# Optimization experiments

Measured on AMD Instinct MI355X. Metric: run time of the kernel, lower is better.

## Reference

```python
import jax, jax.numpy as jnp
import numpy as np

N_NODES = 100000
N_EDGES = 400000
D = 128           # vector_dim
N_GRAPHS = 4096
N_LAYERS = 5
IN_FEAT = 11


def setup_inputs() -> dict:
    key = jax.random.key(0)
    ks = jax.random.split(key, 6)
    x = jax.random.uniform(ks[0], (N_NODES, IN_FEAT), dtype=jnp.float32)
    edge_index = jax.random.randint(ks[1], (2, N_EDGES), 0, N_NODES, dtype=jnp.int64)
    batch = jnp.sort(jax.random.randint(ks[2], (N_NODES,), 0, N_GRAPHS, dtype=jnp.int64))
    # expansion Linear(11, D)
    We = jax.random.normal(ks[3], (IN_FEAT, D), dtype=jnp.float32) * (1.0 / np.sqrt(IN_FEAT))
    be = jnp.zeros((D,), dtype=jnp.float32)
    # stacked GCNConv weights/biases for 5 layers
    Wg = jax.random.normal(ks[4], (N_LAYERS, D, D), dtype=jnp.float32) * (1.0 / np.sqrt(D))
    bg = jnp.zeros((N_LAYERS, D), dtype=jnp.float32)
    return {"x": x, "edge_index": edge_index, "batch": batch, "num_graphs": N_GRAPHS,
            "We": We, "be": be, "Wg": Wg, "bg": bg}


def reference(x, edge_index, batch, num_graphs, We, be, Wg, bg):
    n = x.shape[0]
    src, dst = edge_index[0], edge_index[1]
    # GCNConv(improved=True): self-loop weight 2 -> deg[i] = in_degree + 2
    deg = jax.ops.segment_sum(jnp.ones((src.shape[0],), x.dtype), dst, num_segments=n) + 2.0
    dinv = deg ** -0.5
    enorm = dinv[src] * dinv[dst]          # per-edge symmetric norm [E]
    self_norm = 2.0 * dinv * dinv          # self-loop contribution [N]

    h = jnp.log(x + 1.0) @ We + be         # expansion [N, D]
    for l in range(Wg.shape[0]):
        t = h @ Wg[l]                      # [N, D]
        agg = jax.ops.segment_sum(t[src] * enorm[:, None], dst, num_segments=n)
        agg = agg + self_norm[:, None] * t + bg[l]
        h = h + jax.nn.relu(agg)           # residual; dropout = identity (eval)
    return jax.ops.segment_sum(h, batch, num_segments=num_graphs)  # global_add_pool [G, D]
```

## Files before the change

### kernel.cpp

```cpp
#include <hip/hip_runtime.h>
#include <hip/hip_bf16.h>

#define NN 100000
#define NE 400000
#define DD 128
#define NG 4096
#define NL 5
#define NF 11


__global__ void deg_kernel(const int* __restrict__ ei, int* __restrict__ deg) {
    int e = blockIdx.x * 256 + threadIdx.x;
    if (e < NE) atomicAdd(&deg[ei[NE + e]], 1);
}

__global__ void scan1_kernel(const int* __restrict__ deg, int* __restrict__ off,
                             int* __restrict__ bsums) {
    __shared__ int lds[256];
    int tid = threadIdx.x, b = blockIdx.x;
    int base = b * 1024 + tid * 4;
    int v[4];
#pragma unroll
    for (int q = 0; q < 4; ++q) {
        int i = base + q;
        v[q] = (i < NN) ? deg[i] : 0;
    }
    int s = v[0] + v[1] + v[2] + v[3];
    lds[tid] = s;
    __syncthreads();
    for (int o = 1; o < 256; o <<= 1) {
        int t2 = (tid >= o) ? lds[tid - o] : 0;
        __syncthreads();
        lds[tid] += t2;
        __syncthreads();
    }
    int p = lds[tid] - s;
#pragma unroll
    for (int q = 0; q < 4; ++q) {
        int i = base + q;
        if (i < NN) off[i] = p;
        p += v[q];
    }
    if (tid == 255) bsums[b] = lds[255];
}

__global__ void scan2_kernel(int* __restrict__ bsums, int nb) {
    __shared__ int lds[128];
    int tid = threadIdx.x;
    int v = (tid < nb) ? bsums[tid] : 0;
    lds[tid] = v;
    __syncthreads();
    for (int o = 1; o < 128; o <<= 1) {
        int t2 = (tid >= o) ? lds[tid - o] : 0;
        __syncthreads();
        lds[tid] += t2;
        __syncthreads();
    }
    if (tid < nb) bsums[tid] = lds[tid] - v;
}

__global__ void finish_kernel(int* __restrict__ off, const int* __restrict__ bsums,
                              const int* __restrict__ deg, float* __restrict__ dinv) {
    int i = blockIdx.x * 256 + threadIdx.x;
    if (i == 0) off[NN] = NE;
    if (i < NN) {
        off[i] += bsums[i >> 10];
        dinv[i] = rsqrtf((float)deg[i] + 2.0f);
    }
}

__global__ void fill_kernel(const int* __restrict__ ei, const int* __restrict__ off,
                            int* __restrict__ cursor, int2* __restrict__ csr,
                            const float* __restrict__ dinv) {
    int e = blockIdx.x * 256 + threadIdx.x;
    if (e >= NE) return;
    int s = ei[e];
    int d = ei[NE + e];
    int pos = off[d] + atomicAdd(&cursor[d], 1);
    csr[pos] = make_int2(s, __float_as_int(dinv[s] * dinv[d]));
}


__global__ void expand_kernel(const float* __restrict__ x, const float* __restrict__ We,
                              const float* __restrict__ be, float* __restrict__ h) {
    int t = blockIdx.x * 256 + threadIdx.x;
    int i = t >> 7, j = t & 127;
    float acc = be[j];
#pragma unroll
    for (int f = 0; f < NF; ++f) {
        acc += __logf(x[i * NF + f] + 1.0f) * We[f * DD + j];
    }
    h[t] = acc;
}


__global__ __launch_bounds__(256) void layer_kernel(const float* __restrict__ hin,
                                                    float* __restrict__ hout,
                                                    const int* __restrict__ off,
                                                    const int2* __restrict__ csr,
                                                    const float* __restrict__ dinv,
                                                    const float* __restrict__ W,
                                                    const float* __restrict__ b) {
    __shared__ float gs[64 * 132];
    __shared__ float ws[2][8 * 128];
    const int tid = threadIdx.x;
    const int node0 = blockIdx.x * 64;
    const float4* __restrict__ h4 = (const float4*)hin;

    const int jj = tid & 31;
    const int sub = tid >> 5;
#pragma unroll 1
    for (int p = 0; p < 8; ++p) {
        const int nl = p * 8 + sub;
        const int node = node0 + nl;
        float4 acc = make_float4(0.f, 0.f, 0.f, 0.f);
        if (node < NN) {
            float di = dinv[node];
            float sn = 2.0f * di * di;
            float4 hv = h4[(size_t)node * 32 + jj];
            acc = make_float4(sn * hv.x, sn * hv.y, sn * hv.z, sn * hv.w);
            int e = off[node];
            const int e1 = off[node + 1];
            for (; e + 4 <= e1; e += 4) {
                int2 p0 = csr[e], p1 = csr[e + 1], p2 = csr[e + 2], p3 = csr[e + 3];
                float4 v0 = h4[(size_t)p0.x * 32 + jj];
                float4 v1 = h4[(size_t)p1.x * 32 + jj];
                float4 v2 = h4[(size_t)p2.x * 32 + jj];
                float4 v3 = h4[(size_t)p3.x * 32 + jj];
                float w0 = __int_as_float(p0.y), w1 = __int_as_float(p1.y);
                float w2 = __int_as_float(p2.y), w3 = __int_as_float(p3.y);
                acc.x = fmaf(w0, v0.x, acc.x); acc.y = fmaf(w0, v0.y, acc.y);
                acc.z = fmaf(w0, v0.z, acc.z); acc.w = fmaf(w0, v0.w, acc.w);
                acc.x = fmaf(w1, v1.x, acc.x); acc.y = fmaf(w1, v1.y, acc.y);
                acc.z = fmaf(w1, v1.z, acc.z); acc.w = fmaf(w1, v1.w, acc.w);
                acc.x = fmaf(w2, v2.x, acc.x); acc.y = fmaf(w2, v2.y, acc.y);
                acc.z = fmaf(w2, v2.z, acc.z); acc.w = fmaf(w2, v2.w, acc.w);
                acc.x = fmaf(w3, v3.x, acc.x); acc.y = fmaf(w3, v3.y, acc.y);
                acc.z = fmaf(w3, v3.z, acc.z); acc.w = fmaf(w3, v3.w, acc.w);
            }
            for (; e < e1; ++e) {
                int2 pe = csr[e];
                float4 v = h4[(size_t)pe.x * 32 + jj];
                float w = __int_as_float(pe.y);
                acc.x = fmaf(w, v.x, acc.x); acc.y = fmaf(w, v.y, acc.y);
                acc.z = fmaf(w, v.z, acc.z); acc.w = fmaf(w, v.w, acc.w);
            }
        }
        *(float4*)&gs[nl * 132 + jj * 4] = acc;
    }

    {
        float4 wv = *(const float4*)(W + tid * 4);
        *(float4*)&ws[0][tid * 4] = wv;
    }

    const int cg = tid & 15;
    const int rg = tid >> 4;
    float acc[4][8];
#pragma unroll
    for (int m = 0; m < 4; ++m)
#pragma unroll
        for (int q = 0; q < 8; ++q) acc[m][q] = 0.f;

#pragma unroll 1
    for (int kc = 0; kc < 16; ++kc) {
        const int cur = kc & 1;
        float4 wnext;
        const bool have = (kc + 1 < 16);
        if (have) wnext = *(const float4*)(W + (kc + 1) * 1024 + tid * 4);
        __syncthreads();
#pragma unroll
        for (int kk = 0; kk < 8; ++kk) {
            const float* wrow = &ws[cur][kk * 128];
            float4 wlo = *(const float4*)(wrow + cg * 4);
            float4 whi = *(const float4*)(wrow + cg * 4 + 64);
            const int k = kc * 8 + kk;
#pragma unroll
            for (int m = 0; m < 4; ++m) {
                float gv = gs[(rg + (m << 4)) * 132 + k];
                acc[m][0] = fmaf(gv, wlo.x, acc[m][0]);
                acc[m][1] = fmaf(gv, wlo.y, acc[m][1]);
                acc[m][2] = fmaf(gv, wlo.z, acc[m][2]);
                acc[m][3] = fmaf(gv, wlo.w, acc[m][3]);
                acc[m][4] = fmaf(gv, whi.x, acc[m][4]);
                acc[m][5] = fmaf(gv, whi.y, acc[m][5]);
                acc[m][6] = fmaf(gv, whi.z, acc[m][6]);
                acc[m][7] = fmaf(gv, whi.w, acc[m][7]);
            }
        }
        if (have) *(float4*)&ws[cur ^ 1][tid * 4] = wnext;
    }

    float4 blo = *(const float4*)(b + cg * 4);
    float4 bhi = *(const float4*)(b + cg * 4 + 64);
#pragma unroll
    for (int m = 0; m < 4; ++m) {
        int r = rg + (m << 4);
        int row = node0 + r;
        if (row < NN) {
            size_t o = (size_t)row * DD + cg * 4;
            float4 hlo = *(const float4*)(hin + o);
            float4 hhi = *(const float4*)(hin + o + 64);
            hlo.x += fmaxf(acc[m][0] + blo.x, 0.f);
            hlo.y += fmaxf(acc[m][1] + blo.y, 0.f);
            hlo.z += fmaxf(acc[m][2] + blo.z, 0.f);
            hlo.w += fmaxf(acc[m][3] + blo.w, 0.f);
            hhi.x += fmaxf(acc[m][4] + bhi.x, 0.f);
            hhi.y += fmaxf(acc[m][5] + bhi.y, 0.f);
            hhi.z += fmaxf(acc[m][6] + bhi.z, 0.f);
            hhi.w += fmaxf(acc[m][7] + bhi.w, 0.f);
            *(float4*)(hout + o) = hlo;
            *(float4*)(hout + o + 64) = hhi;
        }
    }
}


__global__ void pool_kernel(const float* __restrict__ h, const int* __restrict__ batch,
                            float* __restrict__ out) {
    int j = threadIdx.x;
    int n0 = blockIdx.x * 64;
    float acc = 0.f;
    int prev = -1;
    for (int n = 0; n < 64; ++n) {
        int i = n0 + n;
        if (i >= NN) break;
        int bi = batch[i];
        if (bi != prev) {
            if (prev >= 0) atomicAdd(&out[(size_t)prev * DD + j], acc);
            acc = 0.f;
            prev = bi;
        }
        acc += h[(size_t)i * DD + j];
    }
    if (prev >= 0) atomicAdd(&out[(size_t)prev * DD + j], acc);
}


static inline size_t align_up(size_t x, size_t a) { return (x + a - 1) & ~(a - 1); }

extern "C" void kernel_launch(void* const* d_in, const int* in_sizes, int n_in,
                              void* d_out, int out_size, void* d_ws, size_t ws_size,
                              hipStream_t stream) {
    const float* x   = (const float*)d_in[0];
    const int*   ei  = (const int*)d_in[1];
    const int*   bat = (const int*)d_in[2];
    const float* We  = (const float*)d_in[4];
    const float* be  = (const float*)d_in[5];
    const float* Wg  = (const float*)d_in[6];
    const float* bg  = (const float*)d_in[7];
    float* out = (float*)d_out;

    char* p = (char*)d_ws;
    size_t o = 0;
    float* h0 = (float*)(p + o);      o = align_up(o + (size_t)NN * DD * 4, 512);
    float* h1 = (float*)(p + o);      o = align_up(o + (size_t)NN * DD * 4, 512);
    float* dinv = (float*)(p + o);    o = align_up(o + (size_t)NN * 4, 512);
    int* deg = (int*)(p + o);         o = align_up(o + (size_t)NN * 4, 512);
    int* cursor = (int*)(p + o);      o = align_up(o + (size_t)NN * 4, 512);
    int* off = (int*)(p + o);         o = align_up(o + (size_t)(NN + 1) * 4, 512);
    int* bsums = (int*)(p + o);       o = align_up(o + 512, 512);
    int2* csr = (int2*)(p + o);       o = align_up(o + (size_t)NE * 8, 512);
    (void)ws_size; (void)in_sizes; (void)n_in; (void)out_size;

    float* hbuf[2] = {h0, h1};

    const int GRID_E = (NE + 255) / 256;
    const int GRID_SCAN1 = (NN + 1023) / 1024;
    const int GRID_N256 = (NN + 255) / 256;
    const int GRID_ND = (size_t)NN * DD / 256;
    const int GRID_LAYER = (NN + 63) / 64;
    const int GRID_POOL = (NN + 63) / 64;

    hipMemsetAsync(deg, 0, (size_t)NN * 4, stream);
    hipMemsetAsync(cursor, 0, (size_t)NN * 4, stream);
    hipMemsetAsync(out, 0, (size_t)NG * DD * 4, stream);

    deg_kernel<<<GRID_E, 256, 0, stream>>>(ei, deg);
    scan1_kernel<<<GRID_SCAN1, 256, 0, stream>>>(deg, off, bsums);
    scan2_kernel<<<1, 128, 0, stream>>>(bsums, GRID_SCAN1);
    finish_kernel<<<GRID_N256, 256, 0, stream>>>(off, bsums, deg, dinv);
    fill_kernel<<<GRID_E, 256, 0, stream>>>(ei, off, cursor, csr, dinv);

    expand_kernel<<<GRID_ND, 256, 0, stream>>>(x, We, be, h0);

    for (int l = 0; l < NL; ++l) {
        const float* hin = hbuf[l & 1];
        float* hout = hbuf[(l & 1) ^ 1];
        layer_kernel<<<GRID_LAYER, 256, 0, stream>>>(hin, hout, off, csr, dinv,
                                                     Wg + (size_t)l * DD * DD,
                                                     bg + (size_t)l * DD);
    }

    pool_kernel<<<GRID_POOL, 128, 0, stream>>>(hbuf[NL & 1], bat, out);
}
```

Baseline: 670.5 us.

## Flatten block edge range for gather with LDS atomic accumulation

The gather phase changes from one 32-thread group per destination node, walking that node's edges with float4 loads, to a flat loop over the block's whole contiguous CSR edge range. Each thread handles one scalar feature of one edge and accumulates into shared memory with atomicAdd. The local destination row is packed into the high bits of the CSR source index. This is meant to fix load imbalance from uneven node degrees, but it trades vector loads for scalar loads, adds LDS atomics, and limits source indices to 24 bits. The W staging tile is also halved so the padded gs buffer fits, with a stride of 129.

```diff
diff --git a/kernel.cpp b/kernel.cpp
--- a/kernel.cpp
+++ b/kernel.cpp
@@ -77,7 +77,7 @@
     int s = ei[e];
     int d = ei[NE + e];
     int pos = off[d] + atomicAdd(&cursor[d], 1);
-    csr[pos] = make_int2(s, __float_as_int(dinv[s] * dinv[d]));
+    csr[pos] = make_int2(s | ((d & 63) << 24), __float_as_int(dinv[s] * dinv[d]));
 }
 
 
@@ -101,57 +101,49 @@
                                                     const float* __restrict__ dinv,
                                                     const float* __restrict__ W,
                                                     const float* __restrict__ b) {
-    __shared__ float gs[64 * 132];
-    __shared__ float ws[2][8 * 128];
+    __shared__ float gs[64 * 129];
+    __shared__ float ws[2][4 * 128];
     const int tid = threadIdx.x;
     const int node0 = blockIdx.x * 64;
-    const float4* __restrict__ h4 = (const float4*)hin;
-
-    const int jj = tid & 31;
-    const int sub = tid >> 5;
-#pragma unroll 1
-    for (int p = 0; p < 8; ++p) {
-        const int nl = p * 8 + sub;
-        const int node = node0 + nl;
-        float4 acc = make_float4(0.f, 0.f, 0.f, 0.f);
+
+#pragma unroll
+    for (int it = 0; it < 32; ++it) {
+        int t = it * 256 + tid;
+        int nl = t >> 7, j = t & 127;
+        int node = node0 + nl;
+        float v = 0.f;
         if (node < NN) {
             float di = dinv[node];
-            float sn = 2.0f * di * di;
-            float4 hv = h4[(size_t)node * 32 + jj];
-            acc = make_float4(sn * hv.x, sn * hv.y, sn * hv.z, sn * hv.w);
-            int e = off[node];
-            const int e1 = off[node + 1];
-            for (; e + 4 <= e1; e += 4) {
-                int2 p0 = csr[e], p1 = csr[e + 1], p2 = csr[e + 2], p3 = csr[e + 3];
-                float4 v0 = h4[(size_t)p0.x * 32 + jj];
-                float4 v1 = h4[(size_t)p1.x * 32 + jj];
-                float4 v2 = h4[(size_t)p2.x * 32 + jj];
-                float4 v3 = h4[(size_t)p3.x * 32 + jj];
-                float w0 = __int_as_float(p0.y), w1 = __int_as_float(p1.y);
-                float w2 = __int_as_float(p2.y), w3 = __int_as_float(p3.y);
-                acc.x = fmaf(w0, v0.x, acc.x); acc.y = fmaf(w0, v0.y, acc.y);
-                acc.z = fmaf(w0, v0.z, acc.z); acc.w = fmaf(w0, v0.w, acc.w);
-                acc.x = fmaf(w1, v1.x, acc.x); acc.y = fmaf(w1, v1.y, acc.y);
-                acc.z = fmaf(w1, v1.z, acc.z); acc.w = fmaf(w1, v1.w, acc.w);
-                acc.x = fmaf(w2, v2.x, acc.x); acc.y = fmaf(w2, v2.y, acc.y);
-                acc.z = fmaf(w2, v2.z, acc.z); acc.w = fmaf(w2, v2.w, acc.w);
-                acc.x = fmaf(w3, v3.x, acc.x); acc.y = fmaf(w3, v3.y, acc.y);
-                acc.z = fmaf(w3, v3.z, acc.z); acc.w = fmaf(w3, v3.w, acc.w);
-            }
-            for (; e < e1; ++e) {
-                int2 pe = csr[e];
-                float4 v = h4[(size_t)pe.x * 32 + jj];
-                float w = __int_as_float(pe.y);
-                acc.x = fmaf(w, v.x, acc.x); acc.y = fmaf(w, v.y, acc.y);
-                acc.z = fmaf(w, v.z, acc.z); acc.w = fmaf(w, v.w, acc.w);
-            }
-        }
-        *(float4*)&gs[nl * 132 + jj * 4] = acc;
-    }
+            v = 2.f * di * di * hin[(size_t)node * DD + j];
+        }
+        gs[nl * 129 + j] = v;
+    }
+    __syncthreads();
 
     {
-        float4 wv = *(const float4*)(W + tid * 4);
-        *(float4*)&ws[0][tid * 4] = wv;
+        const int eLo = off[node0];
+        const int eHi = off[min(node0 + 64, NN)];
+        const int lim = (eHi - eLo) * 128;
+#pragma unroll 1
+        for (int t0 = tid; t0 < lim; t0 += 1024) {
+            int t1 = t0 + 256, t2 = t0 + 512, t3 = t0 + 768;
+            int2 r0, r1, r2, r3;
+            float v0 = 0.f, v1 = 0.f, v2 = 0.f, v3 = 0.f;
+            r0 = csr[eLo + (t0 >> 7)];
+            v0 = hin[(size_t)(r0.x & 0xFFFFFF) * DD + (t0 & 127)];
+            if (t1 < lim) { r1 = csr[eLo + (t1 >> 7)]; v1 = hin[(size_t)(r1.x & 0xFFFFFF) * DD + (t1 & 127)]; }
+            if (t2 < lim) { r2 = csr[eLo + (t2 >> 7)]; v2 = hin[(size_t)(r2.x & 0xFFFFFF) * DD + (t2 & 127)]; }
+            if (t3 < lim) { r3 = csr[eLo + (t3 >> 7)]; v3 = hin[(size_t)(r3.x & 0xFFFFFF) * DD + (t3 & 127)]; }
+            atomicAdd(&gs[((r0.x >> 24) & 63) * 129 + (t0 & 127)], __int_as_float(r0.y) * v0);
+            if (t1 < lim) atomicAdd(&gs[((r1.x >> 24) & 63) * 129 + (t1 & 127)], __int_as_float(r1.y) * v1);
+            if (t2 < lim) atomicAdd(&gs[((r2.x >> 24) & 63) * 129 + (t2 & 127)], __int_as_float(r2.y) * v2);
+            if (t3 < lim) atomicAdd(&gs[((r3.x >> 24) & 63) * 129 + (t3 & 127)], __int_as_float(r3.y) * v3);
+        }
+    }
+
+    {
+        float2 wv = *(const float2*)(W + tid * 2);
+        *(float2*)&ws[0][tid * 2] = wv;
     }
 
     const int cg = tid & 15;
@@ -163,21 +155,21 @@
         for (int q = 0; q < 8; ++q) acc[m][q] = 0.f;
 
 #pragma unroll 1
-    for (int kc = 0; kc < 16; ++kc) {
+    for (int kc = 0; kc < 32; ++kc) {
         const int cur = kc & 1;
-        float4 wnext;
-        const bool have = (kc + 1 < 16);
-        if (have) wnext = *(const float4*)(W + (kc + 1) * 1024 + tid * 4);
-        __syncthreads();
-#pragma unroll
-        for (int kk = 0; kk < 8; ++kk) {
+        float2 wnext;
+        const bool have = (kc + 1 < 32);
+        if (have) wnext = *(const float2*)(W + (kc + 1) * 512 + tid * 2);
+        __syncthreads();
+#pragma unroll
+        for (int kk = 0; kk < 4; ++kk) {
             const float* wrow = &ws[cur][kk * 128];
             float4 wlo = *(const float4*)(wrow + cg * 4);
             float4 whi = *(const float4*)(wrow + cg * 4 + 64);
-            const int k = kc * 8 + kk;
+            const int k = kc * 4 + kk;
 #pragma unroll
             for (int m = 0; m < 4; ++m) {
-                float gv = gs[(rg + (m << 4)) * 132 + k];
+                float gv = gs[(rg + (m << 4)) * 129 + k];
                 acc[m][0] = fmaf(gv, wlo.x, acc[m][0]);
                 acc[m][1] = fmaf(gv, wlo.y, acc[m][1]);
                 acc[m][2] = fmaf(gv, wlo.z, acc[m][2]);
@@ -188,7 +180,7 @@
                 acc[m][7] = fmaf(gv, whi.w, acc[m][7]);
             }
         }
-        if (have) *(float4*)&ws[cur ^ 1][tid * 4] = wnext;
+        if (have) *(float2*)&ws[cur ^ 1][tid * 2] = wnext;
     }
 
     float4 blo = *(const float4*)(b + cg * 4);
```

Result: slower. 1.924 ms (+187.0%).

## Read GCN weights directly from global memory and mask gather-loop tail

Applied to the files above, without the earlier changes.

The double-buffered LDS staging of the layer weight matrix is removed; the dense transform now reads W rows straight from global memory (via the caches), and the gathered-feature tile uses a row stride of 129 instead of 132. The neighbour-gather loop always processes four edges per step, clamping indices and zeroing weights past the end, so the scalar remainder loop goes away. The aim is to cut LDS use and barriers and to simplify control flow. The cost is repeated global or cache reads of W, wasted loads on padded edges, and float4 LDS stores at addresses that are no longer 16-byte aligned.

```diff
diff --git a/kernel.cpp b/kernel.cpp
--- a/kernel.cpp
+++ b/kernel.cpp
@@ -101,8 +101,7 @@
                                                     const float* __restrict__ dinv,
                                                     const float* __restrict__ W,
                                                     const float* __restrict__ b) {
-    __shared__ float gs[64 * 132];
-    __shared__ float ws[2][8 * 128];
+    __shared__ float gs[64 * 129];
     const int tid = threadIdx.x;
     const int node0 = blockIdx.x * 64;
     const float4* __restrict__ h4 = (const float4*)hin;
@@ -119,16 +118,21 @@
             float sn = 2.0f * di * di;
             float4 hv = h4[(size_t)node * 32 + jj];
             acc = make_float4(sn * hv.x, sn * hv.y, sn * hv.z, sn * hv.w);
-            int e = off[node];
+            const int e0 = off[node];
             const int e1 = off[node + 1];
-            for (; e + 4 <= e1; e += 4) {
-                int2 p0 = csr[e], p1 = csr[e + 1], p2 = csr[e + 2], p3 = csr[e + 3];
+#pragma unroll 1
+            for (int e = e0; e < e1; e += 4) {
+                const int eL = e1 - 1;
+                int i1 = min(e + 1, eL), i2 = min(e + 2, eL), i3 = min(e + 3, eL);
+                int2 p0 = csr[e], p1 = csr[i1], p2 = csr[i2], p3 = csr[i3];
                 float4 v0 = h4[(size_t)p0.x * 32 + jj];
                 float4 v1 = h4[(size_t)p1.x * 32 + jj];
                 float4 v2 = h4[(size_t)p2.x * 32 + jj];
                 float4 v3 = h4[(size_t)p3.x * 32 + jj];
-                float w0 = __int_as_float(p0.y), w1 = __int_as_float(p1.y);
-                float w2 = __int_as_float(p2.y), w3 = __int_as_float(p3.y);
+                float w0 = __int_as_float(p0.y);
+                float w1 = (e + 1 < e1) ? __int_as_float(p1.y) : 0.f;
+                float w2 = (e + 2 < e1) ? __int_as_float(p2.y) : 0.f;
+                float w3 = (e + 3 < e1) ? __int_as_float(p3.y) : 0.f;
                 acc.x = fmaf(w0, v0.x, acc.x); acc.y = fmaf(w0, v0.y, acc.y);
                 acc.z = fmaf(w0, v0.z, acc.z); acc.w = fmaf(w0, v0.w, acc.w);
                 acc.x = fmaf(w1, v1.x, acc.x); acc.y = fmaf(w1, v1.y, acc.y);
@@ -138,21 +142,10 @@
                 acc.x = fmaf(w3, v3.x, acc.x); acc.y = fmaf(w3, v3.y, acc.y);
                 acc.z = fmaf(w3, v3.z, acc.z); acc.w = fmaf(w3, v3.w, acc.w);
             }
-            for (; e < e1; ++e) {
-                int2 pe = csr[e];
-                float4 v = h4[(size_t)pe.x * 32 + jj];
-                float w = __int_as_float(pe.y);
-                acc.x = fmaf(w, v.x, acc.x); acc.y = fmaf(w, v.y, acc.y);
-                acc.z = fmaf(w, v.z, acc.z); acc.w = fmaf(w, v.w, acc.w);
-            }
-        }
-        *(float4*)&gs[nl * 132 + jj * 4] = acc;
-    }
-
-    {
-        float4 wv = *(const float4*)(W + tid * 4);
-        *(float4*)&ws[0][tid * 4] = wv;
-    }
+        }
+        *(float4*)&gs[nl * 129 + jj * 4] = acc;
+    }
+    __syncthreads();
 
     const int cg = tid & 15;
     const int rg = tid >> 4;
@@ -162,33 +155,22 @@
 #pragma unroll
         for (int q = 0; q < 8; ++q) acc[m][q] = 0.f;
 
-#pragma unroll 1
-    for (int kc = 0; kc < 16; ++kc) {
-        const int cur = kc & 1;
-        float4 wnext;
-        const bool have = (kc + 1 < 16);
-        if (have) wnext = *(const float4*)(W + (kc + 1) * 1024 + tid * 4);
-        __syncthreads();
-#pragma unroll
-        for (int kk = 0; kk < 8; ++kk) {
-            const float* wrow = &ws[cur][kk * 128];
-            float4 wlo = *(const float4*)(wrow + cg * 4);
-            float4 whi = *(const float4*)(wrow + cg * 4 + 64);
-            const int k = kc * 8 + kk;
-#pragma unroll
-            for (int m = 0; m < 4; ++m) {
-                float gv = gs[(rg + (m << 4)) * 132 + k];
-                acc[m][0] = fmaf(gv, wlo.x, acc[m][0]);
-                acc[m][1] = fmaf(gv, wlo.y, acc[m][1]);
-                acc[m][2] = fmaf(gv, wlo.z, acc[m][2]);
-                acc[m][3] = fmaf(gv, wlo.w, acc[m][3]);
-                acc[m][4] = fmaf(gv, whi.x, acc[m][4]);
-                acc[m][5] = fmaf(gv, whi.y, acc[m][5]);
-                acc[m][6] = fmaf(gv, whi.z, acc[m][6]);
-                acc[m][7] = fmaf(gv, whi.w, acc[m][7]);
-            }
-        }
-        if (have) *(float4*)&ws[cur ^ 1][tid * 4] = wnext;
+#pragma unroll 8
+    for (int k = 0; k < 128; ++k) {
+        float4 wlo = *(const float4*)(W + k * 128 + cg * 4);
+        float4 whi = *(const float4*)(W + k * 128 + cg * 4 + 64);
+#pragma unroll
+        for (int m = 0; m < 4; ++m) {
+            float gv = gs[(rg + (m << 4)) * 129 + k];
+            acc[m][0] = fmaf(gv, wlo.x, acc[m][0]);
+            acc[m][1] = fmaf(gv, wlo.y, acc[m][1]);
+            acc[m][2] = fmaf(gv, wlo.z, acc[m][2]);
+            acc[m][3] = fmaf(gv, wlo.w, acc[m][3]);
+            acc[m][4] = fmaf(gv, whi.x, acc[m][4]);
+            acc[m][5] = fmaf(gv, whi.y, acc[m][5]);
+            acc[m][6] = fmaf(gv, whi.z, acc[m][6]);
+            acc[m][7] = fmaf(gv, whi.w, acc[m][7]);
+        }
     }
 
     float4 blo = *(const float4*)(b + cg * 4);
```

Measured after the change: 655.4 us. 2.3% less time.
